# Kernel tuning notes

Hardware: AMD Instinct MI355X
Metric: run time of the kernel (lower is better)

Reference implementation:

```python
import jax, jax.numpy as jnp
import numpy as np

B, CIN, COUT, K, KN, HID, HW = 16, 256, 256, 3, 4, 16, 64
PAD = K // 2
EPS = 1e-5


def setup_inputs() -> dict:
    key = jax.random.key(0)
    ks = jax.random.split(key, 6)
    x = jax.random.normal(ks[0], (B, CIN, HW, HW), dtype=jnp.float32)
    # attention MLP: 1x1 conv -> BN -> ReLU -> 1x1 conv (on 1x1 pooled maps == dense)
    w1 = jax.random.normal(ks[1], (HID, CIN), dtype=jnp.float32) * (1.0 / np.sqrt(CIN))
    bn_gamma = jnp.ones((HID,), dtype=jnp.float32)
    bn_beta = jnp.zeros((HID,), dtype=jnp.float32)
    bn_mean = jnp.zeros((HID,), dtype=jnp.float32)
    bn_var = jnp.ones((HID,), dtype=jnp.float32)
    w2 = jax.random.normal(ks[2], (KN, HID), dtype=jnp.float32) * (1.0 / np.sqrt(HID))
    # kaiming-normal fan_out: std = sqrt(2 / (Cout * k * k))
    weight = jax.random.normal(ks[3], (KN, COUT, CIN, K, K), dtype=jnp.float32) * np.sqrt(2.0 / (COUT * K * K))
    return {"x": x, "w1": w1, "bn_gamma": bn_gamma, "bn_beta": bn_beta,
            "bn_mean": bn_mean, "bn_var": bn_var, "w2": w2, "weight": weight}


def reference(x, w1, bn_gamma, bn_beta, bn_mean, bn_var, w2, weight):
    b = x.shape[0]
    # global average pool -> [B, Cin]
    pooled = jnp.mean(x, axis=(2, 3))
    h = pooled @ w1.T                                   # [B, HID]
    h = (h - bn_mean) * jax.lax.rsqrt(bn_var + EPS) * bn_gamma + bn_beta
    h = jax.nn.relu(h)
    att = jax.nn.softmax(h @ w2.T, axis=1)              # [B, KN]
    # aggregate per-sample kernels: [B, Cout, Cin, K, K]
    agg_w = jnp.einsum('bk,koijl->boijl', att, weight)
    # batched dynamic conv via batch-as-groups grouped conv
    x_g = x.reshape(1, b * CIN, x.shape[2], x.shape[3])
    w_g = agg_w.reshape(b * COUT, CIN, K, K)
    out = jax.lax.conv_general_dilated(
        x_g, w_g, window_strides=(1, 1), padding=[(PAD, PAD), (PAD, PAD)],
        dimension_numbers=('NCHW', 'OIHW', 'NCHW'), feature_group_count=b)
    return out.reshape(b, COUT, out.shape[2], out.shape[3])
```

## Files before the change

### kernel.cpp

```cpp
#include <hip/hip_runtime.h>

typedef __attribute__((ext_vector_type(8))) short bf16x8;
typedef __attribute__((ext_vector_type(4))) float f32x4;

#define AS3 __attribute__((address_space(3)))
#define AS1 __attribute__((address_space(1)))

__device__ __forceinline__ unsigned short f2bf(float f) {
  unsigned u = __float_as_uint(f);
  u += 0x7fffu + ((u >> 16) & 1u);
  return (unsigned short)(u >> 16);
}
__device__ __forceinline__ float bf2f(unsigned short v) {
  return __uint_as_float((unsigned)v << 16);
}

__global__ void transpose_kernel(const float* __restrict__ x,
                                 unsigned short* __restrict__ xTp,
                                 float* __restrict__ part) {
  __shared__ unsigned short tb[64][258];
  __shared__ float redf[4][256];
  const int blk = blockIdx.x;
  const int b = blk >> 6, y = blk & 63;
  const int t = threadIdx.x;
  const int l = t & 63, w = t >> 6;
  const int coff = l >> 4;
  const int x4 = (l & 15) << 2;
  const float* src = x + (size_t)b * 256 * 4096 + (size_t)y * 64;
#pragma unroll 4
  for (int i = 0; i < 16; ++i) {
    const int c = w * 64 + i * 4 + coff;
    const float4 v = *reinterpret_cast<const float4*>(&src[(size_t)c * 4096 + x4]);
    tb[x4 + 0][c] = f2bf(v.x);
    tb[x4 + 1][c] = f2bf(v.y);
    tb[x4 + 2][c] = f2bf(v.z);
    tb[x4 + 3][c] = f2bf(v.w);
  }
  __syncthreads();
  unsigned short* dstb = xTp + (size_t)b * (4356 * 256);
  unsigned short* dst = dstb + ((size_t)(y + 1) * 66 + 1) * 256;
  float s0 = 0.f, s1 = 0.f, s2 = 0.f, s3 = 0.f;
#pragma unroll 4
  for (int i = 0; i < 16; ++i) {
    const int xx = w * 16 + i;
    ushort2 v0 = *(const ushort2*)&tb[xx][l * 4];
    ushort2 v1 = *(const ushort2*)&tb[xx][l * 4 + 2];
    s0 += bf2f(v0.x); s1 += bf2f(v0.y); s2 += bf2f(v1.x); s3 += bf2f(v1.y);
    ushort4 v = {v0.x, v0.y, v1.x, v1.y};
    *(ushort4*)&dst[(size_t)xx * 256 + l * 4] = v;
  }
  redf[w][l * 4 + 0] = s0;
  redf[w][l * 4 + 1] = s1;
  redf[w][l * 4 + 2] = s2;
  redf[w][l * 4 + 3] = s3;
  unsigned short* rowpad = dstb + ((size_t)(y + 1) * 66) * 256;
  rowpad[t] = 0;
  rowpad[65 * 256 + t] = 0;
  if (y == 0)
    for (int xx = 0; xx < 66; ++xx) dstb[(size_t)xx * 256 + t] = 0;
  if (y == 63)
    for (int xx = 0; xx < 66; ++xx) dstb[(size_t)(65 * 66 + xx) * 256 + t] = 0;
  __syncthreads();
  part[((size_t)(b * 64 + y)) * 256 + t] =
      redf[0][t] + redf[1][t] + redf[2][t] + redf[3][t];
}

__global__ void poolfin_kernel(const float* __restrict__ part,
                               float* __restrict__ pooled) {
  const int b = blockIdx.x, c = threadIdx.x;
  float s = 0.f;
  for (int y = 0; y < 64; ++y) s += part[((size_t)(b * 64 + y)) * 256 + c];
  pooled[b * 256 + c] = s * (1.0f / 4096.0f);
}

__global__ void attn_kernel(const float* __restrict__ pooled,
                            const float* __restrict__ w1,
                            const float* __restrict__ bng,
                            const float* __restrict__ bnb,
                            const float* __restrict__ bnm,
                            const float* __restrict__ bnv,
                            const float* __restrict__ w2,
                            float* __restrict__ att) {
  __shared__ float hbuf[256];
  const int t = threadIdx.x;
  const int b = t >> 4, i = t & 15;
  float s = 0.f;
  for (int c = 0; c < 256; ++c) s += pooled[b * 256 + c] * w1[i * 256 + c];
  float h = (s - bnm[i]) * rsqrtf(bnv[i] + 1e-5f) * bng[i] + bnb[i];
  hbuf[t] = fmaxf(h, 0.f);
  __syncthreads();
  if (t < 64) {
    const int bb = t >> 2, k = t & 3;
    float l = 0.f;
    for (int j = 0; j < 16; ++j) l += hbuf[bb * 16 + j] * w2[k * 16 + j];
    float m = l;
    m = fmaxf(m, __shfl_xor(m, 1, 64));
    m = fmaxf(m, __shfl_xor(m, 2, 64));
    float e = expf(l - m);
    float sum = e;
    sum += __shfl_xor(sum, 1, 64);
    sum += __shfl_xor(sum, 2, 64);
    att[bb * 4 + k] = e / sum;
  }
}

__global__ void agg_kernel(const float* __restrict__ att,
                           const float* __restrict__ wgt,
                           unsigned short* __restrict__ agg) {
  const int o = blockIdx.x;
  const int bh = blockIdx.y;
  const int c = threadIdx.x;
  float w[4][9];
#pragma unroll
  for (int k = 0; k < 4; ++k) {
    const float* wp = wgt + ((size_t)((k << 8) + o) * 256 + c) * 9;
#pragma unroll
    for (int t = 0; t < 9; ++t) w[k][t] = wp[t];
  }
  __shared__ float attS[64];
  if (c < 64) attS[c] = att[c];
  __syncthreads();
#pragma unroll 1
  for (int b = bh * 8; b < bh * 8 + 8; ++b) {
    const float a0 = attS[b * 4 + 0], a1 = attS[b * 4 + 1];
    const float a2 = attS[b * 4 + 2], a3 = attS[b * 4 + 3];
#pragma unroll
    for (int t = 0; t < 9; ++t) {
      const float v = a0 * w[0][t] + a1 * w[1][t] + a2 * w[2][t] + a3 * w[3][t];
      agg[(((size_t)(b * 9 + t) * 256) + o) * 256 + c] = f2bf(v);
    }
  }
}

__global__ __launch_bounds__(256, 2) void conv_kernel(
    const unsigned short* __restrict__ xTp,
    const unsigned short* __restrict__ agg,
    float* __restrict__ out) {
  __shared__ unsigned short lds[(2 * 448 * 32 + 2 * 128 * 32)];

  const int bid = blockIdx.x;
  const int b = bid & 15;
  const int rest = bid >> 4;
  const int mt = rest >> 1;
  const int nh = rest & 1;
  const int p0 = mt << 8;
  const int rowA0 = mt * 264;

  const int tid = threadIdx.x;
  const int lane = tid & 63;
  const int wave = tid >> 6;
  const int wm = wave >> 1;
  const int wn = wave & 1;

  const int srow = tid >> 2;
  const int scol = ((tid & 3) ^ ((tid >> 3) & 3)) << 3;
  const int sdst = srow * 64 + (tid & 3) * 16;

  const unsigned short* xbs =
      xTp + (size_t)b * (4356 * 256) + (size_t)rowA0 * 256 + scol;
  const unsigned short* aggs =
      agg + ((size_t)(b * 9) * 256 + nh * 128 + srow) * 256 + scol;
  AS3 char* ldsA3 = (AS3 char*)lds;
  AS3 char* ldsB3 = ((AS3 char*)lds) + 57344;

  auto stageA = [&](int c0s, int bufo) {
#pragma unroll
    for (int i = 0; i < 7; ++i) {
      const int h = srow + (i << 6);
      const int hs = h > 395 ? 395 : h;
      __builtin_amdgcn_global_load_lds(
          (const AS1 void*)(xbs + (size_t)hs * 256 + c0s * 32),
          (AS3 void*)(ldsA3 + bufo + sdst + (i << 12)), 16, 0, 0);
    }
  };
  auto stageB = [&](int c02, int tap2, int slot) {
#pragma unroll
    for (int j = 0; j < 2; ++j) {
      __builtin_amdgcn_global_load_lds(
          (const AS1 void*)(aggs + tap2 * 65536 + (j << 14) + c02 * 32),
          (AS3 void*)(ldsB3 + slot * 8192 + sdst + (j << 12)), 16, 0, 0);
    }
  };

  const int l15 = lane & 15;
  const int lhi = lane >> 4;
  const int hb0 = wm * 132 + l15;
  const int rslotB = (lhi ^ ((l15 >> 1) & 3)) << 4;
  int boffs[4];
#pragma unroll
  for (int n = 0; n < 4; ++n)
    boffs[n] = 57344 + (wn * 64 + n * 16 + l15) * 64 + rslotB;

  f32x4 acc[8][4];
#pragma unroll
  for (int m = 0; m < 8; ++m)
#pragma unroll
    for (int n = 0; n < 4; ++n) acc[m][n] = (f32x4){0.f, 0.f, 0.f, 0.f};

#define RDA(reg, mm, tt)                                                      \
  {                                                                           \
    const int h_ = hb0 + (((mm) >> 2) + (tt) / 3) * 66 + ((mm)&3) * 16 + (tt) % 3; \
    reg = *(const bf16x8*)((const char*)lds + bufb + h_ * 64 +                \
                           ((lhi ^ ((h_ >> 1) & 3)) << 4));                   \
  }
#define RDB(reg, nn, tt)                                                      \
  reg = *(const bf16x8*)((const char*)lds + (((c0 + (tt)) & 1) << 13) + boffs[nn]);
#define MF4(areg, ii)                                                         \
  acc[ii][0] = __builtin_amdgcn_mfma_f32_16x16x32_bf16(areg, b0, acc[ii][0], 0, 0, 0); \
  acc[ii][1] = __builtin_amdgcn_mfma_f32_16x16x32_bf16(areg, b1, acc[ii][1], 0, 0, 0); \
  acc[ii][2] = __builtin_amdgcn_mfma_f32_16x16x32_bf16(areg, b2, acc[ii][2], 0, 0, 0); \
  acc[ii][3] = __builtin_amdgcn_mfma_f32_16x16x32_bf16(areg, b3, acc[ii][3], 0, 0, 0);
#define STB(tt)                                                               \
  {                                                                           \
    int c02_ = c0 + ((tt) + 2) / 9, tap2_ = ((tt) + 2) % 9;                   \
    if (c02_ > 7) { c02_ = 7; tap2_ = 8; }                                    \
    stageB(c02_, tap2_, (c0 + (tt)) & 1);                                     \
  }
#define TAPBODY(tt, VMC)                                                      \
  {                                                                           \
    asm volatile("s_waitcnt vmcnt(" VMC ")" ::: "memory");                    \
    __builtin_amdgcn_s_barrier();                                             \
    __builtin_amdgcn_sched_barrier(0);                                        \
    bf16x8 a0, a1, a2, a3, a4, a5, a6, a7, b0, b1, b2, b3;                    \
    RDA(a0, 0, tt) RDA(a1, 1, tt) RDA(a2, 2, tt) RDA(a3, 3, tt)               \
    RDB(b0, 0, tt) RDB(b1, 1, tt) RDB(b2, 2, tt) RDB(b3, 3, tt)               \
    __builtin_amdgcn_s_setprio(1);                                            \
    MF4(a0, 0) MF4(a1, 1) MF4(a2, 2) MF4(a3, 3)                               \
    __builtin_amdgcn_s_setprio(0);                                            \
    __builtin_amdgcn_s_barrier();     \
    __builtin_amdgcn_sched_barrier(0);                                        \
    STB(tt);                                                                  \
    if ((tt) == 0) stageA(c0 < 7 ? c0 + 1 : 7, bufb ^ 28672);                 \
    RDA(a4, 4, tt) RDA(a5, 5, tt) RDA(a6, 6, tt) RDA(a7, 7, tt)               \
    __builtin_amdgcn_s_setprio(1);                                            \
    MF4(a4, 4) MF4(a5, 5) MF4(a6, 6) MF4(a7, 7)                               \
    __builtin_amdgcn_s_setprio(0);                                            \
  }

  stageA(0, 0);
  stageB(0, 0, 0);
  stageB(0, 1, 1);
  asm volatile("s_waitcnt vmcnt(0)" ::: "memory");
  __builtin_amdgcn_s_barrier();

#pragma unroll 1
  for (int c0 = 0; c0 < 8; ++c0) {
    const int bufb = (c0 & 1) * 28672;
    TAPBODY(0, "2")
    TAPBODY(1, "9")
    TAPBODY(2, "9")
    TAPBODY(3, "2")
    TAPBODY(4, "2")
    TAPBODY(5, "2")
    TAPBODY(6, "2")
    TAPBODY(7, "2")
    TAPBODY(8, "2")
  }

#pragma unroll
  for (int m = 0; m < 8; ++m) {
    const int p = p0 + wm * 128 + (m >> 2) * 64 + (m & 3) * 16 + (lhi << 2);
#pragma unroll
    for (int n = 0; n < 4; ++n) {
      const int co = nh * 128 + wn * 64 + n * 16 + l15;
      float* dst = out + ((size_t)(b * 256 + co) << 12) + p;
      *reinterpret_cast<f32x4*>(dst) = acc[m][n];
    }
  }
#undef RDA
#undef RDB
#undef MF4
#undef STB
#undef TAPBODY
}

extern "C" void kernel_launch(void* const* d_in, const int* in_sizes, int n_in,
                              void* d_out, int out_size, void* d_ws, size_t ws_size,
                              hipStream_t stream) {
  const float* x = (const float*)d_in[0];
  const float* w1 = (const float*)d_in[1];
  const float* bng = (const float*)d_in[2];
  const float* bnb = (const float*)d_in[3];
  const float* bnm = (const float*)d_in[4];
  const float* bnv = (const float*)d_in[5];
  const float* w2 = (const float*)d_in[6];
  const float* wgt = (const float*)d_in[7];
  float* out = (float*)d_out;

  char* ws = (char*)d_ws;
  const size_t xtp_bytes = (size_t)16 * 4356 * 256 * 2;
  const size_t agg_bytes = (size_t)16 * 9 * 256 * 256 * 2;
  unsigned short* xTp = (unsigned short*)ws;
  unsigned short* agg = (unsigned short*)(ws + xtp_bytes);
  float* pooled = (float*)(ws + xtp_bytes + agg_bytes);
  float* att = (float*)(ws + xtp_bytes + agg_bytes + 16384);
  float* part = (float*)(ws + xtp_bytes + agg_bytes + 20480);

  transpose_kernel<<<1024, 256, 0, stream>>>(x, xTp, part);
  poolfin_kernel<<<16, 256, 0, stream>>>(part, pooled);
  attn_kernel<<<1, 256, 0, stream>>>(pooled, w1, bng, bnb, bnm, bnv, w2, att);
  agg_kernel<<<dim3(256, 2), 256, 0, stream>>>(att, wgt, agg);
  conv_kernel<<<512, 256, 0, stream>>>(xTp, agg, out);
}
```

Baseline: 130.6 us.

## Software-pipeline conv mainloop with register double-buffering and triple-buffered B tiles

Restructures the conv main loop into a flat 72-step loop over (channel chunk, tap), handled two steps per iteration. A and B fragments are double-buffered in registers so the LDS reads for the next half-step overlap the current MFMAs. The B staging ring grows from two to three slots. The A-tile prefetch is spread as one row-chunk per tap instead of a burst at tap 0. This aims to hide LDS and global load latency behind MFMA work, at the cost of more registers, more LDS and tighter vmcnt/barrier ordering that must stay correct.

```diff
diff --git a/kernel.cpp b/kernel.cpp
--- a/kernel.cpp
+++ b/kernel.cpp
@@ -136,7 +136,7 @@
     const unsigned short* __restrict__ xTp,
     const unsigned short* __restrict__ agg,
     float* __restrict__ out) {
-  __shared__ unsigned short lds[(2 * 448 * 32 + 2 * 128 * 32)];
+  __shared__ unsigned short lds[40960];
 
   const int bid = blockIdx.x;
   const int b = bid & 15;
@@ -173,23 +173,33 @@
           (AS3 void*)(ldsA3 + bufo + sdst + (i << 12)), 16, 0, 0);
     }
   };
-  auto stageB = [&](int c02, int tap2, int slot) {
+  auto stageB = [&](int c02, int tap2, int slotb) {
 #pragma unroll
     for (int j = 0; j < 2; ++j) {
       __builtin_amdgcn_global_load_lds(
           (const AS1 void*)(aggs + tap2 * 65536 + (j << 14) + c02 * 32),
-          (AS3 void*)(ldsB3 + slot * 8192 + sdst + (j << 12)), 16, 0, 0);
+          (AS3 void*)(ldsB3 + slotb + sdst + (j << 12)), 16, 0, 0);
     }
+  };
+  auto chunkA = [&](int tapc, int c0cur) {
+    const int i = tapc > 6 ? 6 : tapc;
+    const int c0s = c0cur < 7 ? c0cur + 1 : 7;
+    const int bufo = ((c0cur + 1) & 1) * 28672;
+    const int h = srow + (i << 6);
+    const int hs = h > 395 ? 395 : h;
+    __builtin_amdgcn_global_load_lds(
+        (const AS1 void*)(xbs + (size_t)hs * 256 + c0s * 32),
+        (AS3 void*)(ldsA3 + bufo + sdst + (i << 12)), 16, 0, 0);
   };
 
   const int l15 = lane & 15;
   const int lhi = lane >> 4;
   const int hb0 = wm * 132 + l15;
   const int rslotB = (lhi ^ ((l15 >> 1) & 3)) << 4;
-  int boffs[4];
+  int bo[4];
 #pragma unroll
   for (int n = 0; n < 4; ++n)
-    boffs[n] = 57344 + (wn * 64 + n * 16 + l15) * 64 + rslotB;
+    bo[n] = (wn * 64 + n * 16 + l15) * 64 + rslotB;
 
   f32x4 acc[8][4];
 #pragma unroll
@@ -197,64 +207,99 @@
 #pragma unroll
     for (int n = 0; n < 4; ++n) acc[m][n] = (f32x4){0.f, 0.f, 0.f, 0.f};
 
-#define RDA(reg, mm, tt)                                                      \
-  {                                                                           \
-    const int h_ = hb0 + (((mm) >> 2) + (tt) / 3) * 66 + ((mm)&3) * 16 + (tt) % 3; \
-    reg = *(const bf16x8*)((const char*)lds + bufb + h_ * 64 +                \
-                           ((lhi ^ ((h_ >> 1) & 3)) << 4));                   \
-  }
-#define RDB(reg, nn, tt)                                                      \
-  reg = *(const bf16x8*)((const char*)lds + (((c0 + (tt)) & 1) << 13) + boffs[nn]);
-#define MF4(areg, ii)                                                         \
-  acc[ii][0] = __builtin_amdgcn_mfma_f32_16x16x32_bf16(areg, b0, acc[ii][0], 0, 0, 0); \
-  acc[ii][1] = __builtin_amdgcn_mfma_f32_16x16x32_bf16(areg, b1, acc[ii][1], 0, 0, 0); \
-  acc[ii][2] = __builtin_amdgcn_mfma_f32_16x16x32_bf16(areg, b2, acc[ii][2], 0, 0, 0); \
-  acc[ii][3] = __builtin_amdgcn_mfma_f32_16x16x32_bf16(areg, b3, acc[ii][3], 0, 0, 0);
-#define STB(tt)                                                               \
-  {                                                                           \
-    int c02_ = c0 + ((tt) + 2) / 9, tap2_ = ((tt) + 2) % 9;                   \
-    if (c02_ > 7) { c02_ = 7; tap2_ = 8; }                                    \
-    stageB(c02_, tap2_, (c0 + (tt)) & 1);                                     \
-  }
-#define TAPBODY(tt, VMC)                                                      \
-  {                                                                           \
-    asm volatile("s_waitcnt vmcnt(" VMC ")" ::: "memory");                    \
-    __builtin_amdgcn_s_barrier();                                             \
-    __builtin_amdgcn_sched_barrier(0);                                        \
-    bf16x8 a0, a1, a2, a3, a4, a5, a6, a7, b0, b1, b2, b3;                    \
-    RDA(a0, 0, tt) RDA(a1, 1, tt) RDA(a2, 2, tt) RDA(a3, 3, tt)               \
-    RDB(b0, 0, tt) RDB(b1, 1, tt) RDB(b2, 2, tt) RDB(b3, 3, tt)               \
-    __builtin_amdgcn_s_setprio(1);                                            \
-    MF4(a0, 0) MF4(a1, 1) MF4(a2, 2) MF4(a3, 3)                               \
-    __builtin_amdgcn_s_setprio(0);                                            \
-    __builtin_amdgcn_s_barrier();     \
-    __builtin_amdgcn_sched_barrier(0);                                        \
-    STB(tt);                                                                  \
-    if ((tt) == 0) stageA(c0 < 7 ? c0 + 1 : 7, bufb ^ 28672);                 \
-    RDA(a4, 4, tt) RDA(a5, 5, tt) RDA(a6, 6, tt) RDA(a7, 7, tt)               \
-    __builtin_amdgcn_s_setprio(1);                                            \
-    MF4(a4, 4) MF4(a5, 5) MF4(a6, 6) MF4(a7, 7)                               \
-    __builtin_amdgcn_s_setprio(0);                                            \
-  }
+#define RDA4(DST, HB, BUF, HOFF)                                              \
+  _Pragma("unroll") for (int jj = 0; jj < 4; ++jj) {                          \
+    const int h_ = (HB) + (HOFF) + jj * 16;                                   \
+    DST[jj] = *(const bf16x8*)((const char*)lds + (BUF) + h_ * 64 +           \
+                               ((lhi ^ ((h_ >> 1) & 3)) << 4));               \
+  }
+#define RDB4(DST, SLOTB)                                                      \
+  _Pragma("unroll") for (int nn = 0; nn < 4; ++nn) DST[nn] =                  \
+      *(const bf16x8*)((const char*)lds + 57344 + (SLOTB) + bo[nn]);
+#define MFMA16(AX, BX, R)                                                     \
+  _Pragma("unroll") for (int mm = 0; mm < 4; ++mm)                            \
+  _Pragma("unroll") for (int nn = 0; nn < 4; ++nn)                            \
+      acc[(R) + mm][nn] = __builtin_amdgcn_mfma_f32_16x16x32_bf16(            \
+          AX[mm], BX[nn], acc[(R) + mm][nn], 0, 0, 0);
+
+  bf16x8 A0[4], A1[4], B0[4], B1[4];
 
   stageA(0, 0);
   stageB(0, 0, 0);
-  stageB(0, 1, 1);
+  stageB(0, 1, 8192);
+  stageB(0, 2, 16384);
   asm volatile("s_waitcnt vmcnt(0)" ::: "memory");
   __builtin_amdgcn_s_barrier();
-
+  __builtin_amdgcn_sched_barrier(0);
+  RDA4(A0, hb0, 0, 0);
+  RDB4(B0, 0);
+
+  int ks = 0;
 #pragma unroll 1
-  for (int c0 = 0; c0 < 8; ++c0) {
-    const int bufb = (c0 & 1) * 28672;
-    TAPBODY(0, "2")
-    TAPBODY(1, "9")
-    TAPBODY(2, "9")
-    TAPBODY(3, "2")
-    TAPBODY(4, "2")
-    TAPBODY(5, "2")
-    TAPBODY(6, "2")
-    TAPBODY(7, "2")
-    TAPBODY(8, "2")
+  for (int it = 0; it < 36; ++it) {
+    const int ksE = ks, ksO = ks + 1;
+    const int c0E = (ksE * 57) >> 9, tapE = ksE - c0E * 9;
+    const int c0O = (ksO * 57) >> 9, tapO = ksO - c0O * 9;
+    int ksN = ks + 2;
+    int c0N = (ksN * 57) >> 9, tapN = ksN - c0N * 9;
+    if (ksN > 71) { c0N = 7; tapN = 8; }
+    int ksP = ks + 3;
+    int c0P = (ksP * 57) >> 9, tapP = ksP - c0P * 9;
+    if (ksP > 71) { c0P = 7; tapP = 8; }
+    int ksQ = ks + 4;
+    int c0Q = (ksQ * 57) >> 9, tapQ = ksQ - c0Q * 9;
+    if (ksQ > 71) { c0Q = 7; tapQ = 8; }
+    const int bufE = (c0E & 1) * 28672;
+    const int bufO = (c0O & 1) * 28672;
+    const int bufN = (c0N & 1) * 28672;
+    const int dyE = (tapE * 171) >> 9, dxE = tapE - dyE * 3;
+    const int dyO = (tapO * 171) >> 9, dxO = tapO - dyO * 3;
+    const int dyN = (tapN * 171) >> 9, dxN = tapN - dyN * 3;
+    const int hbE = hb0 + dyE * 66 + dxE;
+    const int hbO = hb0 + dyO * 66 + dxO;
+    const int hbN = hb0 + dyN * 66 + dxN;
+    const int slotO = (ksO % 3) * 8192;
+    const int slotN = (ksN % 3) * 8192;
+    const int slotSE = (ksE % 3) * 8192;
+    const int slotSO = (ksO % 3) * 8192;
+
+    asm volatile("s_waitcnt vmcnt(3)" ::: "memory");
+    __builtin_amdgcn_s_barrier();
+    __builtin_amdgcn_sched_barrier(0);
+    RDA4(A1, hbE, bufE, 66);
+    __builtin_amdgcn_sched_barrier(0);
+    __builtin_amdgcn_s_setprio(1);
+    MFMA16(A0, B0, 0);
+    __builtin_amdgcn_s_setprio(0);
+    __builtin_amdgcn_s_barrier();
+    __builtin_amdgcn_sched_barrier(0);
+    RDA4(A0, hbO, bufO, 0);
+    RDB4(B1, slotO);
+    stageB(c0P, tapP, slotSE);
+    chunkA(tapE, c0E);
+    __builtin_amdgcn_sched_barrier(0);
+    __builtin_amdgcn_s_setprio(1);
+    MFMA16(A1, B0, 4);
+    __builtin_amdgcn_s_setprio(0);
+    asm volatile("s_waitcnt vmcnt(3)" ::: "memory");
+    __builtin_amdgcn_s_barrier();
+    __builtin_amdgcn_sched_barrier(0);
+    RDA4(A1, hbO, bufO, 66);
+    __builtin_amdgcn_sched_barrier(0);
+    __builtin_amdgcn_s_setprio(1);
+    MFMA16(A0, B1, 0);
+    __builtin_amdgcn_s_setprio(0);
+    __builtin_amdgcn_s_barrier();
+    __builtin_amdgcn_sched_barrier(0);
+    RDA4(A0, hbN, bufN, 0);
+    RDB4(B0, slotN);
+    stageB(c0Q, tapQ, slotSO);
+    chunkA(tapO, c0O);
+    __builtin_amdgcn_sched_barrier(0);
+    __builtin_amdgcn_s_setprio(1);
+    MFMA16(A1, B1, 4);
+    __builtin_amdgcn_s_setprio(0);
+    ks += 2;
   }
 
 #pragma unroll
@@ -267,11 +312,9 @@
       *reinterpret_cast<f32x4*>(dst) = acc[m][n];
     }
   }
-#undef RDA
-#undef RDB
-#undef MF4
-#undef STB
-#undef TAPBODY
+#undef RDA4
+#undef RDB4
+#undef MFMA16
 }
 
 extern "C" void kernel_launch(void* const* d_in, const int* in_sizes, int n_in,
```

Result: faster. 113.4 us (-13.1%).
